# Kernel optimization log

Measured on AMD Instinct MI355X. Metric: run time of the kernel, lower is better.

## Reference

```python
import jax, jax.numpy as jnp
import numpy as np

EPS = 1e-5
HEADS = 4
N_SIDE = 32  # im_h == im_w


def _rel_pos_indices(n):
    idx = np.arange(n)
    xi = np.repeat(idx, n)
    yi = np.tile(idx, n)
    pos = np.stack([xi, yi])                      # [2, n^2]
    d = pos[:, None, :] - pos[:, :, None]          # [2, n^2, n^2]
    d = np.clip(d, -n, n) + (n - 1)
    return d[0], d[1]


def _conv1x1(x, W):
    # x: [b,c,H,W], W: [o,c]
    return jnp.einsum('bchw,oc->bohw', x, W)


def _bn(x, g, b, m, v):
    inv = jax.lax.rsqrt(v + EPS)
    return (x - m[:, None, None]) * (inv * g)[:, None, None] + b[:, None, None]


def setup_inputs() -> dict:
    key = jax.random.key(0)
    ks = jax.random.split(key, 8)
    b, dim, H = 16, 256, N_SIDE
    dim_k, heads, dim_out = 16, HEADS, 256
    dim_v = dim_out // heads
    return {
        'x': jax.random.normal(ks[0], (b, dim, H, H), jnp.float32),
        'Wq': jax.random.normal(ks[1], (dim_k * heads, dim), jnp.float32) * 0.05,
        'Wk': jax.random.normal(ks[2], (dim_k, dim), jnp.float32) * 0.05,
        'Wv': jax.random.normal(ks[3], (dim_v, dim), jnp.float32) * 0.05,
        'gq': jnp.ones((dim_k * heads,), jnp.float32),
        'bq': jnp.zeros((dim_k * heads,), jnp.float32),
        'mq': jax.random.normal(ks[4], (dim_k * heads,), jnp.float32) * 0.1,
        'vq': jax.random.uniform(ks[5], (dim_k * heads,), jnp.float32, 0.5, 1.5),
        'gv': jnp.ones((dim_v,), jnp.float32),
        'bv': jnp.zeros((dim_v,), jnp.float32),
        'mv': jax.random.normal(ks[6], (dim_v,), jnp.float32) * 0.1,
        'vv': jax.random.uniform(ks[7], (dim_v,), jnp.float32, 0.5, 1.5),
        'rel_pos_emb': jax.random.normal(jax.random.fold_in(key, 7), (2 * H - 1, 2 * H - 1, dim_k), jnp.float32) * 0.05,
    }


def reference(x, Wq, Wk, Wv, gq, bq, mq, vq, gv, bv, mv, vv, rel_pos_emb):
    b, c, H, W = x.shape
    heads = HEADS
    m = H * W
    dim_k = Wk.shape[0]
    dim_v = Wv.shape[0]

    Q = _bn(_conv1x1(x, Wq), gq, bq, mq, vq)              # [b, h*k, H, W]
    K = _conv1x1(x, Wk)                                   # [b, k, H, W]
    V = _bn(_conv1x1(x, Wv), gv, bv, mv, vv)              # [b, v, H, W]

    Q = Q.reshape(b, heads, dim_k, m).transpose(0, 1, 3, 2)   # [b, h, m, k]
    K = K.reshape(b, dim_k, m).transpose(0, 2, 1)             # [b, m, k]
    V = V.reshape(b, dim_v, m).transpose(0, 2, 1)             # [b, m, v]

    sK = jax.nn.softmax(K, axis=-1)  # NOTE: source softmaxes over k, not m
    lam_c = jnp.einsum('bmk,bmv->bkv', sK, V)
    content = jnp.einsum('bhnk,bkv->bnhv', Q, lam_c)

    r0, r1 = _rel_pos_indices(H)
    emb = rel_pos_emb[r0, r1]                         # [m, m, k]
    lam_p = jnp.einsum('nmk,bmv->bnkv', emb, V)       # [b, m, k, v]
    position = jnp.einsum('bhnk,bnkv->bnhv', Q, lam_p)

    out = content + position                          # [b, m, h, v]
    return out.reshape(b, H, W, heads * dim_v)
```

## Files before the change

### kernel.cpp

```cpp
#include <hip/hip_runtime.h>
#include <math.h>

namespace {
typedef unsigned short u16;
typedef __attribute__((ext_vector_type(4))) float f32x4;
typedef __attribute__((ext_vector_type(8))) short bf16x8;

constexpr int kB  = 16;
constexpr int kC  = 256;
constexpr int kM  = 1024;

__device__ inline u16 f2b(float f) {
    union { float f; unsigned u; } un; un.f = f;
    unsigned r = un.u + 0x7FFF + ((un.u >> 16) & 1);
    return (u16)(r >> 16);
}

__global__ __launch_bounds__(256) void k_prep(
    const float* __restrict__ Wq, const float* __restrict__ Wk,
    const float* __restrict__ Wv,
    const float* __restrict__ gq, const float* __restrict__ bq,
    const float* __restrict__ mq, const float* __restrict__ vq,
    const float* __restrict__ gv, const float* __restrict__ bv,
    const float* __restrict__ mv, const float* __restrict__ vv,
    const float* __restrict__ rpe,
    u16* __restrict__ Wb, float* __restrict__ bb, u16* __restrict__ rpe_b)
{
    const int bid = blockIdx.x;
    const int t = threadIdx.x;
    if (bid < 9) {
        const int oc = bid * 16 + (t >> 4);
        const int c0 = (t & 15) * 16;
        float s, bias;
        const float* wrow;
        if (oc < 64)      { float inv = rsqrtf(vq[oc] + 1e-5f); s = inv * gq[oc]; bias = bq[oc] - mq[oc] * s; wrow = Wq + (size_t)oc * kC; }
        else if (oc < 80) { s = 1.f; bias = 0.f; wrow = Wk + (size_t)(oc - 64) * kC; }
        else              { int i2 = oc - 80; float inv = rsqrtf(vv[i2] + 1e-5f); s = inv * gv[i2]; bias = bv[i2] - mv[i2] * s; wrow = Wv + (size_t)i2 * kC; }
#pragma unroll
        for (int cc = 0; cc < 16; ++cc)
            Wb[(size_t)oc * kC + c0 + cc] = f2b(wrow[c0 + cc] * s);
        if (c0 == 0) bb[oc] = bias;
    } else {
        const int dr = bid - 9;
        for (int e = t; e < 2048; e += 256) {
            int dc = e >> 5, k = e & 31;
            float v = (dc < 63 && k < 16) ? rpe[((size_t)dr * 63 + dc) * 16 + k] : 0.f;
            rpe_b[((size_t)dr * 64 + dc) * 32 + k] = f2b(v);
        }
    }
}

__global__ __launch_bounds__(256) void k_qkv(
    const float* __restrict__ x, const u16* __restrict__ Wb,
    const float* __restrict__ bb,
    u16* __restrict__ Qb, float* __restrict__ Kf, u16* __restrict__ Vb)
{
    __shared__ u16 Xs[16][264];

    const int b  = blockIdx.y;
    const int m0 = blockIdx.x * 16;
    const int t  = threadIdx.x;
    const int w  = t >> 6, lane = t & 63, li = lane & 15, lg = lane >> 4;

#pragma unroll
    for (int j = 0; j < 4; ++j) {
        int e = t + 256 * j;
        int c = e >> 2, m4 = (e & 3) * 4;
        float4 xv = *(const float4*)&x[(size_t)(b * kC + c) * kM + m0 + m4];
        Xs[m4 + 0][c] = f2b(xv.x);
        Xs[m4 + 1][c] = f2b(xv.y);
        Xs[m4 + 2][c] = f2b(xv.z);
        Xs[m4 + 3][c] = f2b(xv.w);
    }
    __syncthreads();

    const int nt = (w == 0) ? 3 : 2;
    const int t0 = (w == 0) ? 0 : 2 * w + 1;

    f32x4 acc[3];
#pragma unroll
    for (int i = 0; i < 3; ++i) acc[i] = (f32x4){0.f, 0.f, 0.f, 0.f};

    for (int ch = 0; ch < 8; ++ch) {
        const int c0 = ch * 32 + lg * 8;
        bf16x8 bfr = *(const bf16x8*)&Xs[li][c0];
        for (int i = 0; i < nt; ++i) {
            bf16x8 afr = *(const bf16x8*)&Wb[(size_t)((t0 + i) * 16 + li) * kC + c0];
            acc[i] = __builtin_amdgcn_mfma_f32_16x16x32_bf16(afr, bfr, acc[i], 0, 0, 0);
        }
    }

    const int m = m0 + li;
    for (int i = 0; i < nt; ++i) {
        const int tile = t0 + i;
        const int ocb = tile * 16 + lg * 4;
        float o[4];
#pragma unroll
        for (int reg = 0; reg < 4; ++reg) o[reg] = acc[i][reg] + bb[ocb + reg];
        if (tile < 4) {
            u16 pk[4];
#pragma unroll
            for (int reg = 0; reg < 4; ++reg) pk[reg] = f2b(o[reg]);
            u16* qp = Qb + ((size_t)(b * 4 + tile) * kM + m) * 32;
            *(uint2*)&qp[lg * 4] = *(const uint2*)pk;
            uint2 z; z.x = 0u; z.y = 0u;
            *(uint2*)&qp[16 + lg * 4] = z;
        } else if (tile == 4) {
#pragma unroll
            for (int reg = 0; reg < 4; ++reg)
                Kf[(size_t)(b * 16 + lg * 4 + reg) * kM + m] = o[reg];
        } else {
            const int vb = (tile - 5) * 16 + lg * 4;
#pragma unroll
            for (int reg = 0; reg < 4; ++reg)
                Vb[(size_t)(b * 64 + vb + reg) * kM + m] = f2b(o[reg]);
        }
    }
}

__global__ __launch_bounds__(512) void k_lam(
    const float* __restrict__ Kf, const u16* __restrict__ Vb,
    u16* __restrict__ lamb)
{
    __shared__ u16 sk[16][1048];
    __shared__ float red[2][4][16][16];

    const int b = blockIdx.x, t = threadIdx.x;

#pragma unroll
    for (int j = 0; j < 2; ++j) {
        const int m = t + 512 * j;
        float vals[16];
        float mx = -1e30f;
#pragma unroll
        for (int k = 0; k < 16; ++k) { vals[k] = Kf[(size_t)(b * 16 + k) * kM + m]; mx = fmaxf(mx, vals[k]); }
        float sum = 0.f;
#pragma unroll
        for (int k = 0; k < 16; ++k) { vals[k] = __expf(vals[k] - mx); sum += vals[k]; }
        const float inv = 1.f / sum;
#pragma unroll
        for (int k = 0; k < 16; ++k) sk[k][m] = f2b(vals[k] * inv);
    }
    __syncthreads();

    const int w = t >> 6, lane = t & 63, li = lane & 15, lg = lane >> 4;
    const int ms = w >> 2, vt = w & 3;
    f32x4 acc = {0.f, 0.f, 0.f, 0.f};
    for (int ck = 0; ck < 16; ++ck) {
        const int mch = ms * 512 + ck * 32 + lg * 8;
        bf16x8 af = *(const bf16x8*)&sk[li][mch];
        bf16x8 bf_ = *(const bf16x8*)&Vb[(size_t)(b * 64 + vt * 16 + li) * kM + mch];
        acc = __builtin_amdgcn_mfma_f32_16x16x32_bf16(af, bf_, acc, 0, 0, 0);
    }
#pragma unroll
    for (int reg = 0; reg < 4; ++reg)
        red[ms][vt][lg * 4 + reg][li] = acc[reg];
    __syncthreads();

    for (int e = t; e < 2048; e += 512) {
        int v = e >> 5, k = e & 31;
        u16 o = 0;
        if (k < 16) o = f2b(red[0][v >> 4][k][v & 15] + red[1][v >> 4][k][v & 15]);
        lamb[(size_t)b * 2048 + v * 32 + k] = o;
    }
}

__global__ __launch_bounds__(256, 2) void k_attn(
    const u16* __restrict__ Qb, const u16* __restrict__ Vb,
    const u16* __restrict__ rpe_b, const u16* __restrict__ lamb,
    float* __restrict__ out)
{
    __shared__ u16 Sl[4][32][72];

    const int b = blockIdx.y, nblk = blockIdx.x, n0 = nblk * 32;
    const int t = threadIdx.x;
    const int h = t >> 6, lane = t & 63, li = lane & 15, lg = lane >> 4;

    const u16* Vbb = Vb + (size_t)b * 64 * kM;
    u16* Sh = &Sl[h][0][0];

    const u16* Qbase = Qb + ((size_t)(b * 4 + h) * kM + n0) * 32;
    bf16x8 qf[2];
    qf[0] = *(const bf16x8*)&Qbase[(size_t)li * 32 + lg * 8];
    qf[1] = *(const bf16x8*)&Qbase[(size_t)(16 + li) * 32 + lg * 8];

    f32x4 acc[2][4];
    const u16* lb = lamb + (size_t)b * 2048;
#pragma unroll
    for (int c = 0; c < 4; ++c) {
        bf16x8 cb = *(const bf16x8*)&lb[(size_t)(16 * c + li) * 32 + lg * 8];
        f32x4 z = {0.f, 0.f, 0.f, 0.f};
        acc[0][c] = __builtin_amdgcn_mfma_f32_16x16x32_bf16(qf[0], cb, z, 0, 0, 0);
        acc[1][c] = __builtin_amdgcn_mfma_f32_16x16x32_bf16(qf[1], cb, z, 0, 0, 0);
    }

    bf16x8 ra[4], vf[4];
    {
        const int dr = 31 - nblk;
#pragma unroll
        for (int g = 0; g < 4; ++g)
            ra[g] = *(const bf16x8*)&rpe_b[((size_t)dr * 64 + g * 16 + li) * 32 + lg * 8];
#pragma unroll
        for (int c = 0; c < 4; ++c)
            vf[c] = *(const bf16x8*)&Vbb[(size_t)(16 * c + li) * kM + lg * 8];
    }

#pragma unroll 2
    for (int mrow = 0; mrow < 32; ++mrow) {
        bf16x8 ran[4], vfn[4];
        if (mrow < 31) {
            const int dr = mrow + 1 - nblk + 31;
            const int mb2 = (mrow + 1) * 32;
#pragma unroll
            for (int g = 0; g < 4; ++g)
                ran[g] = *(const bf16x8*)&rpe_b[((size_t)dr * 64 + g * 16 + li) * 32 + lg * 8];
#pragma unroll
            for (int c = 0; c < 4; ++c)
                vfn[c] = *(const bf16x8*)&Vbb[(size_t)(16 * c + li) * kM + mb2 + lg * 8];
        }

        f32x4 tq[4][2];
#pragma unroll
        for (int g = 0; g < 4; ++g) {
            f32x4 z = {0.f, 0.f, 0.f, 0.f};
            tq[g][0] = __builtin_amdgcn_mfma_f32_16x16x32_bf16(ra[g], qf[0], z, 0, 0, 0);
            tq[g][1] = __builtin_amdgcn_mfma_f32_16x16x32_bf16(ra[g], qf[1], z, 0, 0, 0);
        }

#pragma unroll
        for (int g = 0; g < 4; ++g)
#pragma unroll
            for (int r = 0; r < 2; ++r) {
                u16 pk[4];
#pragma unroll
                for (int reg = 0; reg < 4; ++reg) pk[reg] = f2b(tq[g][r][reg]);
                *(uint2*)&Sh[(size_t)(16 * r + li) * 72 + 16 * g + 4 * lg] = *(const uint2*)pk;
            }

        asm volatile("" ::: "memory");

#pragma unroll
        for (int r = 0; r < 2; ++r) {
            const int base = (16 * r + li) * 72 + 8 * lg + 31 - 16 * r - li;
            bf16x8 sa;
#pragma unroll
            for (int j = 0; j < 8; ++j) sa[j] = (short)Sh[base + j];
            __builtin_amdgcn_s_setprio(1);
#pragma unroll
            for (int c = 0; c < 4; ++c)
                acc[r][c] = __builtin_amdgcn_mfma_f32_16x16x32_bf16(sa, vf[c], acc[r][c], 0, 0, 0);
            __builtin_amdgcn_s_setprio(0);
        }

        if (mrow < 31) {
#pragma unroll
            for (int g = 0; g < 4; ++g) ra[g] = ran[g];
#pragma unroll
            for (int c = 0; c < 4; ++c) vf[c] = vfn[c];
        }
    }

    float* ob = out + ((size_t)b * kM + n0) * 256 + h * 64;
#pragma unroll
    for (int r = 0; r < 2; ++r)
#pragma unroll
        for (int c = 0; c < 4; ++c)
#pragma unroll
            for (int reg = 0; reg < 4; ++reg)
                ob[(size_t)(16 * r + 4 * lg + reg) * 256 + 16 * c + li] = acc[r][c][reg];
}

}

extern "C" void kernel_launch(void* const* d_in, const int* in_sizes, int n_in,
                              void* d_out, int out_size, void* d_ws, size_t ws_size,
                              hipStream_t stream) {
    const float* x   = (const float*)d_in[0];
    const float* Wq  = (const float*)d_in[1];
    const float* Wk  = (const float*)d_in[2];
    const float* Wv  = (const float*)d_in[3];
    const float* gq  = (const float*)d_in[4];
    const float* bq  = (const float*)d_in[5];
    const float* mq  = (const float*)d_in[6];
    const float* vq  = (const float*)d_in[7];
    const float* gv  = (const float*)d_in[8];
    const float* bv  = (const float*)d_in[9];
    const float* mv  = (const float*)d_in[10];
    const float* vv  = (const float*)d_in[11];
    const float* rpe = (const float*)d_in[12];
    float* out = (float*)d_out;

    float* Kf    = (float*)d_ws;
    float* bbuf  = Kf + (size_t)16 * 16 * 1024;
    u16*   Qb    = (u16*)(bbuf + 256);
    u16*   Vb    = Qb + (size_t)16 * 4 * 1024 * 32;
    u16*   rpe_b = Vb + (size_t)16 * 64 * 1024;
    u16*   Wb    = rpe_b + (size_t)63 * 64 * 32;
    u16*   lamb  = Wb + (size_t)144 * 256;

    k_prep<<<72, 256, 0, stream>>>(Wq, Wk, Wv, gq, bq, mq, vq, gv, bv, mv, vv,
                                   rpe, Wb, bbuf, rpe_b);
    k_qkv<<<dim3(64, 16), 256, 0, stream>>>(x, Wb, bbuf, Qb, Kf, Vb);
    k_lam<<<16, 512, 0, stream>>>(Kf, Vb, lamb);
    k_attn<<<dim3(32, 16), 256, 0, stream>>>(Qb, Vb, rpe_b, lamb, out);
}
```

Measured before the change: 162.2 us.

## Split attention m-loop across two wave groups with shared-memory reduction

```diff
diff --git a/kernel.cpp b/kernel.cpp
--- a/kernel.cpp
+++ b/kernel.cpp
@@ -81,6 +81,7 @@
 #pragma unroll
     for (int i = 0; i < 3; ++i) acc[i] = (f32x4){0.f, 0.f, 0.f, 0.f};
 
+#pragma unroll
     for (int ch = 0; ch < 8; ++ch) {
         const int c0 = ch * 32 + lg * 8;
         bf16x8 bfr = *(const bf16x8*)&Xs[li][c0];
@@ -165,50 +166,58 @@
     }
 }
 
-__global__ __launch_bounds__(256, 2) void k_attn(
+__global__ __launch_bounds__(512, 4) void k_attn(
     const u16* __restrict__ Qb, const u16* __restrict__ Vb,
     const u16* __restrict__ rpe_b, const u16* __restrict__ lamb,
     float* __restrict__ out)
 {
-    __shared__ u16 Sl[4][32][72];
+    __shared__ u16 Sl[8][32][72];
+    __shared__ float Red[4][64][33];
 
     const int b = blockIdx.y, nblk = blockIdx.x, n0 = nblk * 32;
     const int t = threadIdx.x;
-    const int h = t >> 6, lane = t & 63, li = lane & 15, lg = lane >> 4;
+    const int wid = t >> 6, lane = t & 63, li = lane & 15, lg = lane >> 4;
+    const int h = wid & 3, mh = wid >> 2;
 
     const u16* Vbb = Vb + (size_t)b * 64 * kM;
-    u16* Sh = &Sl[h][0][0];
+    u16* Sh = &Sl[wid][0][0];
 
     const u16* Qbase = Qb + ((size_t)(b * 4 + h) * kM + n0) * 32;
-    bf16x8 qf[2];
-    qf[0] = *(const bf16x8*)&Qbase[(size_t)li * 32 + lg * 8];
-    qf[1] = *(const bf16x8*)&Qbase[(size_t)(16 + li) * 32 + lg * 8];
+    bf16x8 qf0 = __builtin_nontemporal_load((const bf16x8*)&Qbase[(size_t)li * 32 + lg * 8]);
+    bf16x8 qf1 = __builtin_nontemporal_load((const bf16x8*)&Qbase[(size_t)(16 + li) * 32 + lg * 8]);
 
     f32x4 acc[2][4];
-    const u16* lb = lamb + (size_t)b * 2048;
-#pragma unroll
-    for (int c = 0; c < 4; ++c) {
-        bf16x8 cb = *(const bf16x8*)&lb[(size_t)(16 * c + li) * 32 + lg * 8];
-        f32x4 z = {0.f, 0.f, 0.f, 0.f};
-        acc[0][c] = __builtin_amdgcn_mfma_f32_16x16x32_bf16(qf[0], cb, z, 0, 0, 0);
-        acc[1][c] = __builtin_amdgcn_mfma_f32_16x16x32_bf16(qf[1], cb, z, 0, 0, 0);
-    }
-
+    if (mh == 0) {
+        const u16* lb = lamb + (size_t)b * 2048;
+#pragma unroll
+        for (int c = 0; c < 4; ++c) {
+            bf16x8 cb = *(const bf16x8*)&lb[(size_t)(16 * c + li) * 32 + lg * 8];
+            f32x4 z = {0.f, 0.f, 0.f, 0.f};
+            acc[0][c] = __builtin_amdgcn_mfma_f32_16x16x32_bf16(qf0, cb, z, 0, 0, 0);
+            acc[1][c] = __builtin_amdgcn_mfma_f32_16x16x32_bf16(qf1, cb, z, 0, 0, 0);
+        }
+    } else {
+#pragma unroll
+        for (int r = 0; r < 2; ++r)
+#pragma unroll
+            for (int c = 0; c < 4; ++c) acc[r][c] = (f32x4){0.f, 0.f, 0.f, 0.f};
+    }
+
+    const int lo = mh * 16, hi = lo + 16;
     bf16x8 ra[4], vf[4];
     {
-        const int dr = 31 - nblk;
+        const int dr = lo - nblk + 31;
 #pragma unroll
         for (int g = 0; g < 4; ++g)
             ra[g] = *(const bf16x8*)&rpe_b[((size_t)dr * 64 + g * 16 + li) * 32 + lg * 8];
 #pragma unroll
         for (int c = 0; c < 4; ++c)
-            vf[c] = *(const bf16x8*)&Vbb[(size_t)(16 * c + li) * kM + lg * 8];
-    }
-
-#pragma unroll 2
-    for (int mrow = 0; mrow < 32; ++mrow) {
+            vf[c] = *(const bf16x8*)&Vbb[(size_t)(16 * c + li) * kM + lo * 32 + lg * 8];
+    }
+
+    for (int mrow = lo; mrow < hi; ++mrow) {
         bf16x8 ran[4], vfn[4];
-        if (mrow < 31) {
+        if (mrow + 1 < hi) {
             const int dr = mrow + 1 - nblk + 31;
             const int mb2 = (mrow + 1) * 32;
 #pragma unroll
@@ -223,8 +232,8 @@
 #pragma unroll
         for (int g = 0; g < 4; ++g) {
             f32x4 z = {0.f, 0.f, 0.f, 0.f};
-            tq[g][0] = __builtin_amdgcn_mfma_f32_16x16x32_bf16(ra[g], qf[0], z, 0, 0, 0);
-            tq[g][1] = __builtin_amdgcn_mfma_f32_16x16x32_bf16(ra[g], qf[1], z, 0, 0, 0);
+            tq[g][0] = __builtin_amdgcn_mfma_f32_16x16x32_bf16(ra[g], qf0, z, 0, 0, 0);
+            tq[g][1] = __builtin_amdgcn_mfma_f32_16x16x32_bf16(ra[g], qf1, z, 0, 0, 0);
         }
 
 #pragma unroll
@@ -252,7 +261,7 @@
             __builtin_amdgcn_s_setprio(0);
         }
 
-        if (mrow < 31) {
+        if (mrow + 1 < hi) {
 #pragma unroll
             for (int g = 0; g < 4; ++g) ra[g] = ran[g];
 #pragma unroll
@@ -260,14 +269,29 @@
         }
     }
 
-    float* ob = out + ((size_t)b * kM + n0) * 256 + h * 64;
-#pragma unroll
-    for (int r = 0; r < 2; ++r)
-#pragma unroll
-        for (int c = 0; c < 4; ++c)
-#pragma unroll
-            for (int reg = 0; reg < 4; ++reg)
-                ob[(size_t)(16 * r + 4 * lg + reg) * 256 + 16 * c + li] = acc[r][c][reg];
+    if (mh == 1) {
+#pragma unroll
+        for (int r = 0; r < 2; ++r)
+#pragma unroll
+            for (int c = 0; c < 4; ++c)
+#pragma unroll
+                for (int reg = 0; reg < 4; ++reg)
+                    Red[h][lane][r * 16 + c * 4 + reg] = acc[r][c][reg];
+    }
+    __syncthreads();
+    if (mh == 0) {
+        float* ob = out + ((size_t)b * kM + n0) * 256 + h * 64;
+#pragma unroll
+        for (int r = 0; r < 2; ++r)
+#pragma unroll
+            for (int c = 0; c < 4; ++c)
+#pragma unroll
+                for (int reg = 0; reg < 4; ++reg) {
+                    float v = acc[r][c][reg] + Red[h][lane][r * 16 + c * 4 + reg];
+                    __builtin_nontemporal_store(
+                        v, &ob[(size_t)(16 * r + 4 * lg + reg) * 256 + 16 * c + li]);
+                }
+    }
 }
 
 }
@@ -302,5 +326,5 @@
                                    rpe, Wb, bbuf, rpe_b);
     k_qkv<<<dim3(64, 16), 256, 0, stream>>>(x, Wb, bbuf, Qb, Kf, Vb);
     k_lam<<<16, 512, 0, stream>>>(Kf, Vb, lamb);
-    k_attn<<<dim3(32, 16), 256, 0, stream>>>(Qb, Vb, rpe_b, lamb, out);
-}
+    k_attn<<<dim3(32, 16), 512, 0, stream>>>(Qb, Vb, rpe_b, lamb, out);
+}
```

Measured after the change: 202.5 us. 24.9% more time.
